# Kernel tuning notes

Hardware: AMD Instinct MI355X
Metric: run time of the kernel (lower is better)

Reference implementation:

```python
import jax, jax.numpy as jnp
import numpy as np

N2, S2, M2 = 20000, 16000, 4000   # hop-2 frontier, hop-2 src fanout, hop-2 dst nodes
S1, M1 = 3500, 1024               # hop-1 src fanout, final batch
D_IN, D_H = 128, 128              # input_dim, internal_dim


def setup_inputs() -> dict:
    key = jax.random.key(0)
    ks = jax.random.split(key, 9)
    return {
        "src_nodes": jax.random.normal(ks[0], (N2, D_IN), dtype=jnp.float32),
        "dstsrc2src_1": jax.random.randint(ks[1], (S1,), 0, M2, dtype=jnp.int64),
        "dstsrc2src_2": jax.random.randint(ks[2], (S2,), 0, N2, dtype=jnp.int64),
        "dstsrc2dst_1": jax.random.randint(ks[3], (M1,), 0, M2, dtype=jnp.int64),
        "dstsrc2dst_2": jax.random.randint(ks[4], (M2,), 0, N2, dtype=jnp.int64),
        "dif_mat_1": jax.random.uniform(ks[5], (M1, S1), dtype=jnp.float32),
        "dif_mat_2": jax.random.uniform(ks[6], (M2, S2), dtype=jnp.float32),
        "w1": jax.random.normal(ks[7], (2 * D_IN, D_H), dtype=jnp.float32) * 0.06,
        "w2": jax.random.normal(ks[8], (2 * D_H, D_H), dtype=jnp.float32) * 0.06,
    }


def _mean_aggregate(feats, dstsrc2src, dstsrc2dst, dif_mat, w):
    # gather -> diffusion matmul -> concat -> linear -> relu
    dst_features = feats[dstsrc2dst]               # [M, d]
    src_features = feats[dstsrc2src]               # [S, d]
    aggregated = dif_mat @ src_features            # [M, d]
    concatenated = jnp.concatenate([aggregated, dst_features], axis=1)  # [M, 2d]
    return jax.nn.relu(concatenated @ w)           # [M, d_out]


def reference(src_nodes, dstsrc2src_1, dstsrc2src_2, dstsrc2dst_1,
              dstsrc2dst_2, dif_mat_1, dif_mat_2, w1, w2):
    # GraphSage.call: hop-2 aggregator first (with *_2 inputs), then hop-1.
    x = _mean_aggregate(src_nodes, dstsrc2src_2, dstsrc2dst_2, dif_mat_2, w1)
    x = _mean_aggregate(x, dstsrc2src_1, dstsrc2dst_1, dif_mat_1, w2)
    return x
```

## Files before the change

### kernel.cpp

```cpp
#include <hip/hip_runtime.h>

typedef __bf16 bf16x8 __attribute__((ext_vector_type(8)));
typedef float  f32x4  __attribute__((ext_vector_type(4)));
typedef unsigned short u16;
typedef u16 u16x8 __attribute__((ext_vector_type(8)));

__device__ __forceinline__ u16 f2bf(float f) {
    unsigned u = __builtin_bit_cast(unsigned, f);
    return (u16)((u + 0x7FFFu + ((u >> 16) & 1u)) >> 16);
}

__device__ __forceinline__ bf16x8 cvt8(const float* __restrict__ p) {
    f32x4 v0 = *(const f32x4*)p;
    f32x4 v1 = *(const f32x4*)(p + 4);
    u16x8 h;
    h[0]=f2bf(v0[0]); h[1]=f2bf(v0[1]); h[2]=f2bf(v0[2]); h[3]=f2bf(v0[3]);
    h[4]=f2bf(v1[0]); h[5]=f2bf(v1[1]); h[6]=f2bf(v1[2]); h[7]=f2bf(v1[3]);
    return __builtin_bit_cast(bf16x8, h);
}

__device__ __forceinline__ bf16x8 cvt8_guard(const float* __restrict__ p, int valid) {
    u16x8 h;
#pragma unroll
    for (int j = 0; j < 8; ++j) h[j] = (j < valid) ? f2bf(p[j]) : (u16)0;
    return __builtin_bit_cast(bf16x8, h);
}

__global__ __launch_bounds__(256) void gather_bt(
    const float* __restrict__ feats, const int* __restrict__ idx,
    u16* __restrict__ Bt, int Kcnt, int Kpad)
{
    int g = blockIdx.x * 256 + threadIdx.x;
    if (g >= Kpad * 128) return;
    int n = g & 127;
    int k = g >> 7;
    u16 v = 0;
    if (k < Kcnt) v = f2bf(feats[(size_t)idx[k] * 128 + n]);
    Bt[(size_t)n * Kpad + k] = v;
}

__global__ __launch_bounds__(256) void gemm_bt(
    const float* __restrict__ A, const u16* __restrict__ Bt,
    float* __restrict__ C, int M, int K, int Kpad, int steps_per_split)
{
    const int wid  = threadIdx.x >> 6;
    const int lane = threadIdx.x & 63;
    const int l15  = lane & 15;
    const int lhi  = lane >> 4;

    const int row0 = blockIdx.x * 128 + wid * 32;
    const int total_steps = (K + 31) >> 5;
    int s0 = blockIdx.y * steps_per_split;
    int s1 = s0 + steps_per_split;
    if (s1 > total_steps) s1 = total_steps;
    if (s0 >= s1) return;

    f32x4 acc[2][8];
#pragma unroll
    for (int i = 0; i < 2; ++i)
#pragma unroll
        for (int j = 0; j < 8; ++j) acc[i][j] = (f32x4){0.f, 0.f, 0.f, 0.f};

    const int rA0 = min(row0 + l15,      M - 1);
    const int rA1 = min(row0 + 16 + l15, M - 1);
    const float* __restrict__ a0p = A + (size_t)rA0 * K;
    const float* __restrict__ a1p = A + (size_t)rA1 * K;

    const u16* __restrict__ btl = Bt + (size_t)l15 * Kpad + lhi * 8;

    for (int s = s0; s < s1; ++s) {
        const int k0   = s << 5;
        const int koff = k0 + lhi * 8;

        bf16x8 af[2];
        if (k0 + 32 <= K) {
            af[0] = cvt8(a0p + koff);
            af[1] = cvt8(a1p + koff);
        } else {
            af[0] = cvt8_guard(a0p + koff, K - koff);
            af[1] = cvt8_guard(a1p + koff, K - koff);
        }

        bf16x8 bfr[8];
#pragma unroll
        for (int cf = 0; cf < 8; ++cf)
            bfr[cf] = __builtin_bit_cast(bf16x8,
                *(const u16x8*)(btl + (size_t)cf * 16 * Kpad + k0));

#pragma unroll
        for (int cf = 0; cf < 8; ++cf) {
            acc[0][cf] = __builtin_amdgcn_mfma_f32_16x16x32_bf16(af[0], bfr[cf], acc[0][cf], 0, 0, 0);
            acc[1][cf] = __builtin_amdgcn_mfma_f32_16x16x32_bf16(af[1], bfr[cf], acc[1][cf], 0, 0, 0);
        }
    }

#pragma unroll
    for (int rf = 0; rf < 2; ++rf)
#pragma unroll
        for (int cf = 0; cf < 8; ++cf)
#pragma unroll
            for (int i = 0; i < 4; ++i) {
                int r = row0 + rf * 16 + lhi * 4 + i;
                if (r < M)
                    atomicAdd(C + (size_t)r * 128 + cf * 16 + l15, acc[rf][cf][i]);
            }
}

__global__ __launch_bounds__(256) void dense_relu(
    const float* __restrict__ agg, const float* __restrict__ fsrc,
    const int* __restrict__ didx, const float* __restrict__ w,
    float* __restrict__ out, int M)
{
    __shared__ float sb[32][257];
    const int tid  = threadIdx.x;
    const int row0 = blockIdx.x * 32;

    for (int i = tid; i < 32 * 32; i += 256) {
        int r = i >> 5, c4 = (i & 31) << 2;
        int gr = row0 + r;
        f32x4 v = (f32x4){0.f, 0.f, 0.f, 0.f};
        if (gr < M) v = *(const f32x4*)(agg + (size_t)gr * 128 + c4);
        sb[r][c4 + 0] = v[0]; sb[r][c4 + 1] = v[1];
        sb[r][c4 + 2] = v[2]; sb[r][c4 + 3] = v[3];
    }
    for (int i = tid; i < 32 * 32; i += 256) {
        int r = i >> 5, c4 = (i & 31) << 2;
        int gr = row0 + r;
        int sr = (gr < M) ? didx[gr] : 0;
        f32x4 v = *(const f32x4*)(fsrc + (size_t)sr * 128 + c4);
        sb[r][128 + c4 + 0] = v[0]; sb[r][128 + c4 + 1] = v[1];
        sb[r][128 + c4 + 2] = v[2]; sb[r][128 + c4 + 3] = v[3];
    }
    __syncthreads();

    const int colg = (tid & 15) << 3;
    const int r0l  = (tid >> 4) * 2;
    float acc0[8], acc1[8];
#pragma unroll
    for (int c = 0; c < 8; ++c) { acc0[c] = 0.f; acc1[c] = 0.f; }

    for (int j = 0; j < 256; ++j) {
        f32x4 wa = *(const f32x4*)(w + j * 128 + colg);
        f32x4 wb = *(const f32x4*)(w + j * 128 + colg + 4);
        float a0 = sb[r0l][j];
        float a1 = sb[r0l + 1][j];
#pragma unroll
        for (int c = 0; c < 4; ++c) {
            acc0[c]     += a0 * wa[c];  acc0[c + 4] += a0 * wb[c];
            acc1[c]     += a1 * wa[c];  acc1[c + 4] += a1 * wb[c];
        }
    }

    int gr0 = row0 + r0l;
    if (gr0 < M) {
#pragma unroll
        for (int c = 0; c < 8; ++c)
            out[(size_t)gr0 * 128 + colg + c] = fmaxf(acc0[c], 0.f);
    }
    int gr1 = gr0 + 1;
    if (gr1 < M) {
#pragma unroll
        for (int c = 0; c < 8; ++c)
            out[(size_t)gr1 * 128 + colg + c] = fmaxf(acc1[c], 0.f);
    }
}

extern "C" void kernel_launch(void* const* d_in, const int* in_sizes, int n_in,
                              void* d_out, int out_size, void* d_ws, size_t ws_size,
                              hipStream_t stream)
{
    const float* src_nodes = (const float*)d_in[0];
    const int*   s1idx     = (const int*)d_in[1];
    const int*   s2idx     = (const int*)d_in[2];
    const int*   d1idx     = (const int*)d_in[3];
    const int*   d2idx     = (const int*)d_in[4];
    const float* dif1      = (const float*)d_in[5];
    const float* dif2      = (const float*)d_in[6];
    const float* w1        = (const float*)d_in[7];
    const float* w2        = (const float*)d_in[8];
    float*       out       = (float*)d_out;

    const int S2 = 16000, M2 = 4000, S1 = 3500, M1 = 1024;
    const int K2 = 16000, K1 = 3500;
    const int Kpad2 = 16000;
    const int Kpad1 = 3520;

    char* ws = (char*)d_ws;
    size_t off = 0;
    float* agg2 = (float*)(ws + off); off += (size_t)M2 * 128 * 4;
    float* agg1 = (float*)(ws + off); off += (size_t)M1 * 128 * 4;
    float* x    = (float*)(ws + off); off += (size_t)M2 * 128 * 4;
    u16*   Bt2  = (u16*)(ws + off);   off += (size_t)128 * Kpad2 * 2;
    u16*   Bt1  = (u16*)(ws + off);   off += (size_t)128 * Kpad1 * 2;

    hipMemsetAsync(agg2, 0, (size_t)(M2 + M1) * 128 * 4, stream);

    gather_bt<<<(Kpad2 * 128 + 255) / 256, 256, 0, stream>>>(src_nodes, s2idx, Bt2, S2, Kpad2);

    {
        const int total_steps = (K2 + 31) >> 5;
        const int ksplit = 8;
        const int sps = (total_steps + ksplit - 1) / ksplit;
        dim3 grid((M2 + 127) / 128, ksplit);
        gemm_bt<<<grid, 256, 0, stream>>>(dif2, Bt2, agg2, M2, K2, Kpad2, sps);
    }

    dense_relu<<<(M2 + 31) / 32, 256, 0, stream>>>(agg2, src_nodes, d2idx, w1, x, M2);

    gather_bt<<<(Kpad1 * 128 + 255) / 256, 256, 0, stream>>>(x, s1idx, Bt1, S1, Kpad1);

    {
        const int total_steps = (K1 + 31) >> 5;
        const int ksplit = 32;
        const int sps = (total_steps + ksplit - 1) / ksplit;
        dim3 grid((M1 + 127) / 128, ksplit);
        gemm_bt<<<grid, 256, 0, stream>>>(dif1, Bt1, agg1, M1, K1, Kpad1, sps);
    }

    dense_relu<<<(M1 + 31) / 32, 256, 0, stream>>>(agg1, x, d1idx, w2, out, M1);
}
```

Baseline: 554.8 us.

## Transpose gather through shared memory, shrink GEMM row tile, prefetch A

```diff
diff --git a/kernel.cpp b/kernel.cpp
--- a/kernel.cpp
+++ b/kernel.cpp
@@ -10,76 +10,89 @@
     return (u16)((u + 0x7FFFu + ((u >> 16) & 1u)) >> 16);
 }
 
-__device__ __forceinline__ bf16x8 cvt8(const float* __restrict__ p) {
-    f32x4 v0 = *(const f32x4*)p;
-    f32x4 v1 = *(const f32x4*)(p + 4);
-    u16x8 h;
-    h[0]=f2bf(v0[0]); h[1]=f2bf(v0[1]); h[2]=f2bf(v0[2]); h[3]=f2bf(v0[3]);
-    h[4]=f2bf(v1[0]); h[5]=f2bf(v1[1]); h[6]=f2bf(v1[2]); h[7]=f2bf(v1[3]);
-    return __builtin_bit_cast(bf16x8, h);
-}
-
-__device__ __forceinline__ bf16x8 cvt8_guard(const float* __restrict__ p, int valid) {
-    u16x8 h;
-#pragma unroll
-    for (int j = 0; j < 8; ++j) h[j] = (j < valid) ? f2bf(p[j]) : (u16)0;
-    return __builtin_bit_cast(bf16x8, h);
-}
-
 __global__ __launch_bounds__(256) void gather_bt(
     const float* __restrict__ feats, const int* __restrict__ idx,
     u16* __restrict__ Bt, int Kcnt, int Kpad)
 {
-    int g = blockIdx.x * 256 + threadIdx.x;
-    if (g >= Kpad * 128) return;
-    int n = g & 127;
-    int k = g >> 7;
-    u16 v = 0;
-    if (k < Kcnt) v = f2bf(feats[(size_t)idx[k] * 128 + n]);
-    Bt[(size_t)n * Kpad + k] = v;
+    __shared__ u16 st[128][66];
+    const int tid = threadIdx.x;
+    const int k0  = blockIdx.x * 64;
+
+#pragma unroll
+    for (int r2 = 0; r2 < 64; r2 += 2) {
+        int r = r2 + (tid >> 7);
+        int c = tid & 127;
+        int k = k0 + r;
+        float v = 0.f;
+        if (k < Kcnt) v = feats[(size_t)idx[k] * 128 + c];
+        st[c][r] = f2bf(v);
+    }
+    __syncthreads();
+
+#pragma unroll
+    for (int p = 0; p < 4; ++p) {
+        int n  = p * 32 + (tid >> 3);
+        int kk = (tid & 7) * 8;
+        u16x8 v;
+#pragma unroll
+        for (int j = 0; j < 8; ++j) v[j] = st[n][kk + j];
+        *(u16x8*)(Bt + (size_t)n * Kpad + k0 + kk) = v;
+    }
+}
+
+__device__ __forceinline__ void loadA8(const float* __restrict__ ap, int koff,
+                                       int K, f32x4& a0, f32x4& a1)
+{
+    if (koff + 8 <= K) {
+        a0 = *(const f32x4*)(ap + koff);
+        a1 = *(const f32x4*)(ap + koff + 4);
+    } else {
+#pragma unroll
+        for (int j = 0; j < 4; ++j) {
+            a0[j] = (koff + j     < K) ? ap[koff + j]     : 0.f;
+            a1[j] = (koff + 4 + j < K) ? ap[koff + 4 + j] : 0.f;
+        }
+    }
+}
+
+__device__ __forceinline__ bf16x8 packA(f32x4 a0, f32x4 a1) {
+    u16x8 h;
+    h[0]=f2bf(a0[0]); h[1]=f2bf(a0[1]); h[2]=f2bf(a0[2]); h[3]=f2bf(a0[3]);
+    h[4]=f2bf(a1[0]); h[5]=f2bf(a1[1]); h[6]=f2bf(a1[2]); h[7]=f2bf(a1[3]);
+    return __builtin_bit_cast(bf16x8, h);
 }
 
 __global__ __launch_bounds__(256) void gemm_bt(
     const float* __restrict__ A, const u16* __restrict__ Bt,
-    float* __restrict__ C, int M, int K, int Kpad, int steps_per_split)
+    float* __restrict__ C, int M, int K, int Kpad, int sps)
 {
     const int wid  = threadIdx.x >> 6;
     const int lane = threadIdx.x & 63;
     const int l15  = lane & 15;
     const int lhi  = lane >> 4;
 
-    const int row0 = blockIdx.x * 128 + wid * 32;
-    const int total_steps = (K + 31) >> 5;
-    int s0 = blockIdx.y * steps_per_split;
-    int s1 = s0 + steps_per_split;
-    if (s1 > total_steps) s1 = total_steps;
+    const int row0  = blockIdx.x * 64 + wid * 16;
+    const int total = (K + 31) >> 5;
+    int s0 = blockIdx.y * sps;
+    int s1 = s0 + sps; if (s1 > total) s1 = total;
     if (s0 >= s1) return;
 
-    f32x4 acc[2][8];
-#pragma unroll
-    for (int i = 0; i < 2; ++i)
-#pragma unroll
-        for (int j = 0; j < 8; ++j) acc[i][j] = (f32x4){0.f, 0.f, 0.f, 0.f};
-
-    const int rA0 = min(row0 + l15,      M - 1);
-    const int rA1 = min(row0 + 16 + l15, M - 1);
-    const float* __restrict__ a0p = A + (size_t)rA0 * K;
-    const float* __restrict__ a1p = A + (size_t)rA1 * K;
-
-    const u16* __restrict__ btl = Bt + (size_t)l15 * Kpad + lhi * 8;
+    f32x4 acc[8];
+#pragma unroll
+    for (int j = 0; j < 8; ++j) acc[j] = (f32x4){0.f, 0.f, 0.f, 0.f};
+
+    const int rA = min(row0 + l15, M - 1);
+    const float* __restrict__ ap = A + (size_t)rA * K;
+    const u16*   __restrict__ btl = Bt + (size_t)l15 * Kpad + lhi * 8;
+
+    f32x4 ra0, ra1;
+    loadA8(ap, (s0 << 5) + lhi * 8, K, ra0, ra1);
 
     for (int s = s0; s < s1; ++s) {
-        const int k0   = s << 5;
-        const int koff = k0 + lhi * 8;
-
-        bf16x8 af[2];
-        if (k0 + 32 <= K) {
-            af[0] = cvt8(a0p + koff);
-            af[1] = cvt8(a1p + koff);
-        } else {
-            af[0] = cvt8_guard(a0p + koff, K - koff);
-            af[1] = cvt8_guard(a1p + koff, K - koff);
-        }
+        const int k0 = s << 5;
+
+        f32x4 na0, na1;
+        if (s + 1 < s1) loadA8(ap, ((s + 1) << 5) + lhi * 8, K, na0, na1);
 
         bf16x8 bfr[8];
 #pragma unroll
@@ -87,23 +100,22 @@
             bfr[cf] = __builtin_bit_cast(bf16x8,
                 *(const u16x8*)(btl + (size_t)cf * 16 * Kpad + k0));
 
-#pragma unroll
-        for (int cf = 0; cf < 8; ++cf) {
-            acc[0][cf] = __builtin_amdgcn_mfma_f32_16x16x32_bf16(af[0], bfr[cf], acc[0][cf], 0, 0, 0);
-            acc[1][cf] = __builtin_amdgcn_mfma_f32_16x16x32_bf16(af[1], bfr[cf], acc[1][cf], 0, 0, 0);
+        bf16x8 af = packA(ra0, ra1);
+#pragma unroll
+        for (int cf = 0; cf < 8; ++cf)
+            acc[cf] = __builtin_amdgcn_mfma_f32_16x16x32_bf16(af, bfr[cf], acc[cf], 0, 0, 0);
+
+        ra0 = na0; ra1 = na1;
+    }
+
+#pragma unroll
+    for (int cf = 0; cf < 8; ++cf)
+#pragma unroll
+        for (int i = 0; i < 4; ++i) {
+            int r = row0 + lhi * 4 + i;
+            if (r < M)
+                atomicAdd(C + (size_t)r * 128 + cf * 16 + l15, acc[cf][i]);
         }
-    }
-
-#pragma unroll
-    for (int rf = 0; rf < 2; ++rf)
-#pragma unroll
-        for (int cf = 0; cf < 8; ++cf)
-#pragma unroll
-            for (int i = 0; i < 4; ++i) {
-                int r = row0 + rf * 16 + lhi * 4 + i;
-                if (r < M)
-                    atomicAdd(C + (size_t)r * 128 + cf * 16 + l15, acc[rf][cf][i]);
-            }
 }
 
 __global__ __launch_bounds__(256) void dense_relu(
@@ -195,26 +207,20 @@
 
     hipMemsetAsync(agg2, 0, (size_t)(M2 + M1) * 128 * 4, stream);
 
-    gather_bt<<<(Kpad2 * 128 + 255) / 256, 256, 0, stream>>>(src_nodes, s2idx, Bt2, S2, Kpad2);
+    gather_bt<<<Kpad2 / 64, 256, 0, stream>>>(src_nodes, s2idx, Bt2, S2, Kpad2);
 
     {
-        const int total_steps = (K2 + 31) >> 5;
-        const int ksplit = 8;
-        const int sps = (total_steps + ksplit - 1) / ksplit;
-        dim3 grid((M2 + 127) / 128, ksplit);
-        gemm_bt<<<grid, 256, 0, stream>>>(dif2, Bt2, agg2, M2, K2, Kpad2, sps);
+        dim3 grid((M2 + 63) / 64, 10);
+        gemm_bt<<<grid, 256, 0, stream>>>(dif2, Bt2, agg2, M2, K2, Kpad2, 50);
     }
 
     dense_relu<<<(M2 + 31) / 32, 256, 0, stream>>>(agg2, src_nodes, d2idx, w1, x, M2);
 
-    gather_bt<<<(Kpad1 * 128 + 255) / 256, 256, 0, stream>>>(x, s1idx, Bt1, S1, Kpad1);
+    gather_bt<<<Kpad1 / 64, 256, 0, stream>>>(x, s1idx, Bt1, S1, Kpad1);
 
     {
-        const int total_steps = (K1 + 31) >> 5;
-        const int ksplit = 32;
-        const int sps = (total_steps + ksplit - 1) / ksplit;
-        dim3 grid((M1 + 127) / 128, ksplit);
-        gemm_bt<<<grid, 256, 0, stream>>>(dif1, Bt1, agg1, M1, K1, Kpad1, sps);
+        dim3 grid((M1 + 63) / 64, 22);
+        gemm_bt<<<grid, 256, 0, stream>>>(dif1, Bt1, agg1, M1, K1, Kpad1, 5);
     }
 
     dense_relu<<<(M1 + 31) / 32, 256, 0, stream>>>(agg1, x, d1idx, w2, out, M1);
```

New measurement: 579.0 us. 4.4% more time.
